# Performance work log

Hardware: AMD Instinct MI355X
Metric: run time of the kernel (lower is better)

Reference implementation:

```python
import jax, jax.numpy as jnp
import numpy as np

N, E = 50000, 1600000
D_IN, D_OUT = 256, 64
ALPHA = 0.2        # LeakyReLU slope used on attention logits (self.leakyrelu)
BT_SLOPE = 0.01    # F.leaky_relu default slope inside relu_bt


def _xavier_normal(key, shape, gain):
    fan_in, fan_out = shape[0], shape[1]
    std = gain * np.sqrt(2.0 / (fan_in + fan_out))
    return jax.random.normal(key, shape, dtype=jnp.float32) * std


def relu_bt(x):
    # -threshold(-leaky_relu(x), -t, -t) == min(leaky_relu(x), t), t = ||x||_inf (detached)
    t = jax.lax.stop_gradient(jnp.max(jnp.abs(x)))
    y = jnp.where(x >= 0, x, BT_SLOPE * x)
    return jnp.minimum(y, t)


def setup_inputs() -> dict:
    key = jax.random.key(0)
    k0, k1, k2, k3, k4, k5 = jax.random.split(key, 6)
    inp = jax.random.normal(k0, (N, D_IN), dtype=jnp.float32)
    edge = jax.random.randint(k1, (2, E), 0, N, dtype=jnp.int64)
    W_high = _xavier_normal(k2, (D_IN, D_OUT), 1.414)
    W_low = _xavier_normal(k3, (D_IN, D_OUT), 1.414)
    a_high = _xavier_normal(k4, (1, D_OUT), 1.414)
    a_low = _xavier_normal(k5, (1, D_OUT), 1.414)
    return {"input": inp, "edge": edge, "W_high": W_high, "W_low": W_low,
            "a_high": a_high, "a_low": a_low}


def reference(input, edge, W_high, W_low, a_high, a_low):
    n = input.shape[0]
    src, dst = edge[0], edge[1]

    h_high = relu_bt(input @ W_high)  # [N, D_OUT]
    h_low = relu_bt(input @ W_low)    # [N, D_OUT]

    # a @ (h[src] -/+ h[dst])^T == (a.h)[src] -/+ (a.h)[dst]: compute per-node scalar
    # projections first, then gather scalars per edge (avoids [E, D_OUT] edge features).
    s_high = h_high @ a_high[0]       # [N]
    s_low = h_low @ a_low[0]          # [N]

    def lrelu(x):
        return jnp.where(x >= 0, x, ALPHA * x)

    edge_e_high = jnp.exp(-lrelu(s_high[src] - s_high[dst]))  # [E]
    edge_e_low = jnp.exp(-lrelu(s_low[src] + s_low[dst]))     # [E]
    # dropout p=0.0 -> identity

    # sparse A @ ones -> per-row sum of attention weights
    rowsum_high = jax.ops.segment_sum(edge_e_high, src, num_segments=n)[:, None]
    rowsum_low = jax.ops.segment_sum(edge_e_low, src, num_segments=n)[:, None]

    # sparse A @ h -> weighted aggregation of neighbor features
    hp_high = jax.ops.segment_sum(edge_e_high[:, None] * h_high[dst], src, num_segments=n)
    hp_low = jax.ops.segment_sum(edge_e_low[:, None] * h_low[dst], src, num_segments=n)

    hp_high = hp_high / (rowsum_high + 1e-16)
    hp_low = hp_low / (rowsum_low + 1e-16)

    # concat=True branch
    return relu_bt(jnp.concatenate([hp_high, hp_low], axis=1))  # [N, 2*D_OUT]
```

## Files before the change

### kernel.cpp

```cpp
#include <hip/hip_runtime.h>
#include <hip/hip_bf16.h>
#include <cstdint>

#define NN    50000
#define NE    1600000
#define DIN   256
#define DOUT  64
#define CAPS  96
#define CAPD  95

#define BKT   196
#define BCAP  10240
#define EPB   4096
#define EPT   16
#define NBIN  391
#define MTB   64
#define NGEMM 782
#define CSPL  4

typedef __attribute__((ext_vector_type(8))) short frag8;
typedef __attribute__((ext_vector_type(4))) float fragc;

union PK { __hip_bfloat162 b2; uint32_t u; };
union CH { frag8 v; uint32_t u[4]; };

__device__ __forceinline__ float leaky01(float x) { return x >= 0.f ? x : 0.01f * x; }

__device__ __forceinline__ uint32_t pk2(float lo, float hi) {
  PK p; p.b2 = __float22bfloat162_rn(make_float2(lo, hi)); return p.u;
}

__device__ __forceinline__ int   bcast_i(int v, int lane) {
  return __builtin_amdgcn_readlane(v, lane);
}
__device__ __forceinline__ float bcast_f(float v, int lane) {
  return __int_as_float(__builtin_amdgcn_readlane(__float_as_int(v), lane));
}

__device__ __forceinline__ float bfH(uint32_t u) { return __uint_as_float(u << 16); }
__device__ __forceinline__ float bfL(uint32_t u) { return __uint_as_float(u & 0xffff0000u); }

__global__ __launch_bounds__(256) void prep_kernel(
    const float* __restrict__ Wh, const float* __restrict__ Wl,
    __hip_bfloat16* __restrict__ Wt, int* __restrict__ cursor)
{
  if (blockIdx.x == 0 && threadIdx.x < BKT) cursor[threadIdx.x] = 0;
  int g = blockIdx.x * 256 + threadIdx.x;
  if (g < 2 * DOUT * DIN) {
    int m = g >> 14, rem = g & 16383;
    int n = rem >> 8, k = rem & 255;
    float v = (m ? Wl : Wh)[k * DOUT + n];
    Wt[g] = __float2bfloat16(v);
  }
}

__global__ __launch_bounds__(256) void fused_kernel(
    const float* __restrict__ inp, const __hip_bfloat16* __restrict__ Wt,
    const float* __restrict__ ah, const float* __restrict__ al,
    const int* __restrict__ edge, int* __restrict__ cursor,
    uint32_t* __restrict__ binned, uint32_t* __restrict__ HL,
    float2* __restrict__ ss)
{
  __shared__ __align__(16) char smem[32768];

  const int idx = blockIdx.x;
  const int t = threadIdx.x;

  if (idx < NBIN) {
    uint32_t* stage  = (uint32_t*)smem;
    int*      hist   = (int*)(smem + 16384);
    int*      cur    = (int*)(smem + 17408);
    int*      base_g = (int*)(smem + 18192);
    int*      scan_s = (int*)(smem + 18976);

    const int e0 = idx * EPB;
    uint32_t v[EPT];
#pragma unroll
    for (int i = 0; i < EPT; i++) {
      int e = e0 + i * 256 + t;
      if (e < NE) {
        uint32_t s = (uint32_t)edge[e];
        uint32_t d = (uint32_t)edge[NE + e];
        v[i] = (s << 16) | d;
      } else {
        v[i] = 0xFFFFFFFFu;
      }
    }
    if (t < 256) hist[t] = 0;
    for (int b = t; b < BKT; b += 256) cur[b] = 0;
    __syncthreads();
#pragma unroll
    for (int i = 0; i < EPT; i++) {
      int b = v[i] >> 24;
      if (b < BKT) atomicAdd(&hist[b], 1);
    }
    __syncthreads();
    if (t < 64) {
      int carry = 0;
#pragma unroll
      for (int seg = 0; seg < 4; seg++) {
        int i = seg * 64 + t;
        int h = hist[i];
        int s = h;
#pragma unroll
        for (int off = 1; off < 64; off <<= 1) {
          int o = __shfl_up(s, off);
          if (t >= off) s += o;
        }
        int excl = carry + s - h;
        if (i <= BKT) scan_s[i] = excl;
        carry += bcast_i(s, 63);
      }
    }
    __syncthreads();
    for (int b = t; b < BKT; b += 256) {
      int h = hist[b];
      base_g[b] = h ? atomicAdd(&cursor[b], h) : 0;
    }
    __syncthreads();
#pragma unroll
    for (int i = 0; i < EPT; i++) {
      int b = v[i] >> 24;
      if (b < BKT) {
        int pos = atomicAdd(&cur[b], 1);
        stage[scan_s[b] + pos] = v[i];
      }
    }
    __syncthreads();
    const int total = scan_s[BKT];
    for (int i = t; i < total; i += 256) {
      int lo = 0, hi = BKT - 1;
      while (lo < hi) { int mid = (lo + hi + 1) >> 1; if (scan_s[mid] <= i) lo = mid; else hi = mid - 1; }
      int ofs = base_g[lo] + (i - scan_s[lo]);
      if (ofs < BCAP) binned[(size_t)lo * BCAP + ofs] = stage[i];
    }
    return;
  }

  frag8* asmem = (frag8*)smem;
  const int gid = idx - NBIN;
  const int n0 = gid * MTB;
  const int lane = t & 63;
  const int w = t >> 6;
  const int quad = lane >> 4, nn = lane & 15;

  const frag8* Wt8 = (const frag8*)Wt;
  const int bbase = ((w * 16 + nn) << 5) + quad;
  frag8 bH[8], bL[8];
#pragma unroll
  for (int q = 0; q < 8; q++) {
    bH[q] = Wt8[bbase + (q << 2)];
    bL[q] = Wt8[2048 + bbase + (q << 2)];
  }

  const float4* inp4 = (const float4*)inp;
#pragma unroll
  for (int i = 0; i < 8; i++) {
    int c = i * 256 + t;
    int r = c & 15;
    int cc = c >> 4;
    int qd = cc & 3;
    int wq = cc >> 2;
    int row = ((wq >> 3) << 4) + r;
    int k0 = ((wq & 7) << 5) + (qd << 3);
    int node = n0 + row;
    float4 a0 = make_float4(0.f, 0.f, 0.f, 0.f), a1 = a0;
    if (node < NN) {
      a0 = inp4[(size_t)node * 64 + (k0 >> 2)];
      a1 = inp4[(size_t)node * 64 + (k0 >> 2) + 1];
    }
    CH ch;
    ch.u[0] = pk2(a0.x, a0.y);
    ch.u[1] = pk2(a0.z, a0.w);
    ch.u[2] = pk2(a1.x, a1.y);
    ch.u[3] = pk2(a1.z, a1.w);
    asmem[c] = ch.v;
  }
  __syncthreads();

  fragc accH[4], accL[4];
#pragma unroll
  for (int m = 0; m < 4; m++) {
    accH[m] = (fragc){0.f, 0.f, 0.f, 0.f};
    accL[m] = (fragc){0.f, 0.f, 0.f, 0.f};
  }

#pragma unroll
  for (int q = 0; q < 8; q++) {
#pragma unroll
    for (int mt = 0; mt < 4; mt++) {
      frag8 af = asmem[(mt << 9) + (q << 6) + lane];
      accH[mt] = __builtin_amdgcn_mfma_f32_16x16x32_bf16(af, bH[q], accH[mt], 0, 0, 0);
      accL[mt] = __builtin_amdgcn_mfma_f32_16x16x32_bf16(af, bL[q], accL[mt], 0, 0, 0);
    }
  }
  __syncthreads();

  float* sred = (float*)smem;
  const float ahv = ah[w * 16 + nn];
  const float alv = al[w * 16 + nn];
#pragma unroll
  for (int mt = 0; mt < 4; mt++) {
#pragma unroll
    for (int r = 0; r < 4; r++) {
      int rowb = (mt << 4) + (quad << 2) + r;
      int node = n0 + rowb;
      float hH = leaky01(accH[mt][r]);
      float hL = leaky01(accL[mt][r]);
      if (node < NN) HL[(size_t)node * DOUT + w * 16 + nn] = pk2(hH, hL);
      float pH = hH * ahv, pL = hL * alv;
#pragma unroll
      for (int off = 1; off < 16; off <<= 1) {
        pH += __shfl_xor(pH, off);
        pL += __shfl_xor(pL, off);
      }
      if (nn == 0) {
        sred[rowb * 8 + w]     = pH;
        sred[rowb * 8 + 4 + w] = pL;
      }
    }
  }
  __syncthreads();
  if (t < 64) {
    int node = n0 + t;
    if (node < NN) {
      float sH = sred[t * 8 + 0] + sred[t * 8 + 1] + sred[t * 8 + 2] + sred[t * 8 + 3];
      float sL = sred[t * 8 + 4] + sred[t * 8 + 5] + sred[t * 8 + 6] + sred[t * 8 + 7];
      ss[node] = make_float2(sH, sL);
    }
  }
}

__global__ __launch_bounds__(256) void csr_kernel(
    const uint32_t* __restrict__ binned, const int* __restrict__ cursor,
    int* __restrict__ col)
{
  __shared__ int cnt[64];
  const int b    = blockIdx.x / CSPL;
  const int part = blockIdx.x % CSPL;
  const int t = threadIdx.x;
  if (t < 64) cnt[t] = 0;
  __syncthreads();
  int n = cursor[b]; if (n > BCAP) n = BCAP;
  const uint32_t* eb = binned + (size_t)b * BCAP;
  for (int i = t; i < n; i += 256) {
    uint32_t v = eb[i];
    int src = v >> 16, dst = v & 0xffff;
    int loc = src & 255;
    if ((loc >> 6) == part) {
      int pos = atomicAdd(&cnt[loc & 63], 1);
      if (pos < CAPD) col[(size_t)src * CAPS + 1 + pos] = dst;
    }
  }
  __syncthreads();
  if (t < 64) {
    int node = (b << 8) + (part << 6) + t;
    if (node < NN) {
      int c = cnt[t]; if (c > CAPD) c = CAPD;
      col[(size_t)node * CAPS] = c;
    }
  }
}

__global__ __launch_bounds__(256) void agg_kernel(
    const uint32_t* __restrict__ HL, const float2* __restrict__ ss,
    const int* __restrict__ col, float* __restrict__ out)
{
  int wave = (blockIdx.x * blockDim.x + threadIdx.x) >> 6;
  int lane = threadIdx.x & 63;
  if (wave >= NN) return;
  const int n = wave;
  const int* cl = col + (size_t)n * CAPS;
  int d = cl[0]; if (d > CAPD) d = CAPD;

  const float2 sn = ss[n];

  float accH = 0.f, accL = 0.f, rsH = 0.f, rsL = 0.f;

  for (int base = 0; base < d; base += 64) {
    int m = d - base; if (m > 64) m = 64;
    int   dst_l = 0;
    float eh_l = 0.f, el_l = 0.f;
    if (lane < m) {
      dst_l = cl[1 + base + lane];
      float2 sd = ss[dst_l];
      float xh = sn.x - sd.x;
      xh = (xh >= 0.f) ? xh : 0.2f * xh;
      eh_l = __expf(-xh);
      float xl = sn.y + sd.y;
      xl = (xl >= 0.f) ? xl : 0.2f * xl;
      el_l = __expf(-xl);
    }
    const int mm = (m + 15) & ~15;
    for (int j = 0; j < mm; j += 16) {
      uint32_t u[16]; float eh[16], el[16];
#pragma unroll
      for (int x = 0; x < 16; x++) {
        int dd = bcast_i(dst_l, j + x);
        u[x]  = HL[((uint32_t)dd << 6) + lane];
        eh[x] = bcast_f(eh_l, j + x);
        el[x] = bcast_f(el_l, j + x);
      }
#pragma unroll
      for (int x = 0; x < 16; x++) {
        accH += eh[x] * bfH(u[x]);
        accL += el[x] * bfL(u[x]);
      }
    }
    float rh = eh_l, rl = el_l;
#pragma unroll
    for (int off = 1; off < 64; off <<= 1) {
      rh += __shfl_xor(rh, off);
      rl += __shfl_xor(rl, off);
    }
    rsH += rh; rsL += rl;
  }

  float oh = accH / (rsH + 1e-16f);
  float ol = accL / (rsL + 1e-16f);
  out[(size_t)n * 128 + lane]      = leaky01(oh);
  out[(size_t)n * 128 + 64 + lane] = leaky01(ol);
}

extern "C" void kernel_launch(void* const* d_in, const int* in_sizes, int n_in,
                              void* d_out, int out_size, void* d_ws, size_t ws_size,
                              hipStream_t stream) {
  const float* inp  = (const float*)d_in[0];
  const int*   edge = (const int*)d_in[1];
  const float* Wh   = (const float*)d_in[2];
  const float* Wl   = (const float*)d_in[3];
  const float* ah   = (const float*)d_in[4];
  const float* al   = (const float*)d_in[5];
  float* out = (float*)d_out;

  char* ws = (char*)d_ws;
  uint32_t* HL     = (uint32_t*)(ws + 0);
  float2*   ss     = (float2*)  (ws + 12800000);
  int*      col    = (int*)     (ws + 13200000);
  uint32_t* binned = (uint32_t*)(ws + 32400000);
  int*      cursor = (int*)     (ws + 40428160);
  __hip_bfloat16* Wt = (__hip_bfloat16*)(ws + 13200000);

  prep_kernel<<<128, 256, 0, stream>>>(Wh, Wl, Wt, cursor);
  fused_kernel<<<NBIN + NGEMM, 256, 0, stream>>>(inp, Wt, ah, al, edge,
                                                 cursor, binned, HL, ss);
  csr_kernel<<<BKT * CSPL, 256, 0, stream>>>(binned, cursor, col);
  agg_kernel<<<NN / 4, 256, 0, stream>>>(HL, ss, col, out);
}
```

Measured before the change: 203.6 us.

## Stage CSR rows in shared memory, drop bin search, tighten aggregation loop

The binning scatter now reads each staged edge's bucket from its high byte, replacing the binary search over the prefix scan. The CSR kernel builds each group of 64 nodes' adjacency lists in shared memory and then writes them to global memory with coalesced int4 stores, replacing scattered per-edge global writes. The aggregation kernel switches from padded 16-wide batches to 8-wide batches plus a scalar tail, and accumulates row sums inside the loop instead of using a wave shuffle reduction. These changes cost extra shared memory per CSR block, which may lower occupancy, and the whole padded rows of the column buffer are now written back.

```diff
diff --git a/kernel.cpp b/kernel.cpp
--- a/kernel.cpp
+++ b/kernel.cpp
@@ -129,10 +129,10 @@
     __syncthreads();
     const int total = scan_s[BKT];
     for (int i = t; i < total; i += 256) {
-      int lo = 0, hi = BKT - 1;
-      while (lo < hi) { int mid = (lo + hi + 1) >> 1; if (scan_s[mid] <= i) lo = mid; else hi = mid - 1; }
-      int ofs = base_g[lo] + (i - scan_s[lo]);
-      if (ofs < BCAP) binned[(size_t)lo * BCAP + ofs] = stage[i];
+      uint32_t sv = stage[i];
+      int bb = sv >> 24;
+      int ofs = base_g[bb] + (i - scan_s[bb]);
+      if (ofs < BCAP) binned[(size_t)bb * BCAP + ofs] = sv;
     }
     return;
   }
@@ -235,6 +235,7 @@
     const uint32_t* __restrict__ binned, const int* __restrict__ cursor,
     int* __restrict__ col)
 {
+  __shared__ int lst[64][CAPS];
   __shared__ int cnt[64];
   const int b    = blockIdx.x / CSPL;
   const int part = blockIdx.x % CSPL;
@@ -249,16 +250,21 @@
     int loc = src & 255;
     if ((loc >> 6) == part) {
       int pos = atomicAdd(&cnt[loc & 63], 1);
-      if (pos < CAPD) col[(size_t)src * CAPS + 1 + pos] = dst;
+      if (pos < CAPD) lst[loc & 63][1 + pos] = dst;
     }
   }
   __syncthreads();
   if (t < 64) {
-    int node = (b << 8) + (part << 6) + t;
-    if (node < NN) {
-      int c = cnt[t]; if (c > CAPD) c = CAPD;
-      col[(size_t)node * CAPS] = c;
-    }
+    int c = cnt[t]; if (c > CAPD) c = CAPD;
+    lst[t][0] = c;
+  }
+  __syncthreads();
+  const int base_node = (b << 8) + (part << 6);
+  int4* dst4 = (int4*)(col + (size_t)base_node * CAPS);
+  const int4* src4 = (const int4*)&lst[0][0];
+  for (int i = t; i < 64 * CAPS / 4; i += 256) {
+    int node = base_node + i / (CAPS / 4);
+    if (node < NN) dst4[i] = src4[i];
   }
 }
 
@@ -291,29 +297,32 @@
       xl = (xl >= 0.f) ? xl : 0.2f * xl;
       el_l = __expf(-xl);
     }
-    const int mm = (m + 15) & ~15;
-    for (int j = 0; j < mm; j += 16) {
-      uint32_t u[16]; float eh[16], el[16];
-#pragma unroll
-      for (int x = 0; x < 16; x++) {
+    int j = 0;
+    for (; j + 8 <= m; j += 8) {
+      uint32_t u[8]; float eh[8], el[8];
+#pragma unroll
+      for (int x = 0; x < 8; x++) {
         int dd = bcast_i(dst_l, j + x);
         u[x]  = HL[((uint32_t)dd << 6) + lane];
         eh[x] = bcast_f(eh_l, j + x);
         el[x] = bcast_f(el_l, j + x);
       }
 #pragma unroll
-      for (int x = 0; x < 16; x++) {
-        accH += eh[x] * bfH(u[x]);
-        accL += el[x] * bfL(u[x]);
-      }
-    }
-    float rh = eh_l, rl = el_l;
-#pragma unroll
-    for (int off = 1; off < 64; off <<= 1) {
-      rh += __shfl_xor(rh, off);
-      rl += __shfl_xor(rl, off);
-    }
-    rsH += rh; rsL += rl;
+      for (int x = 0; x < 8; x++) {
+        accH += eh[x] * bfH(u[x]); accL += el[x] * bfL(u[x]);
+        rsH += eh[x]; rsL += el[x];
+      }
+    }
+    for (; j < m; j++) {
+      int      dst = bcast_i(dst_l, j);
+      float    eh  = bcast_f(eh_l, j);
+      float    el  = bcast_f(el_l, j);
+      uint32_t u   = HL[((uint32_t)dst << 6) + lane];
+      accH += eh * bfH(u);
+      accL += el * bfL(u);
+      rsH += eh;
+      rsL += el;
+    }
   }
 
   float oh = accH / (rsH + 1e-16f);
```

After: 198.0 us. -2.7%, faster.
